# Performance work log

Measured on AMD Instinct MI355X. Metric: run time of the kernel, lower is better.

## Reference

```python
import jax, jax.numpy as jnp
import numpy as np

N = 100000
E = 1600000
D_IN, D_HID, D_OUT = 128, 256, 128


def setup_inputs() -> dict:
    key = jax.random.key(0)
    ks = jax.random.split(key, 8)
    x = jax.random.normal(ks[0], (N, D_IN), dtype=jnp.float32)
    edge_index = jax.random.randint(ks[1], (2, E), 0, N, dtype=jnp.int64)
    # PyG SAGEConv params: lin_l (applied to aggregated neighbors, has bias),
    # lin_r (applied to root/self, no bias). Stored as [in, out] for x @ W.
    s0 = 1.0 / np.sqrt(D_IN)
    s1 = 1.0 / np.sqrt(D_HID)
    Wl0 = jax.random.uniform(ks[2], (D_IN, D_HID), jnp.float32, -s0, s0)
    bl0 = jnp.zeros((D_HID,), jnp.float32)
    Wr0 = jax.random.uniform(ks[3], (D_IN, D_HID), jnp.float32, -s0, s0)
    Wl1 = jax.random.uniform(ks[4], (D_HID, D_OUT), jnp.float32, -s1, s1)
    bl1 = jnp.zeros((D_OUT,), jnp.float32)
    Wr1 = jax.random.uniform(ks[5], (D_HID, D_OUT), jnp.float32, -s1, s1)
    return {"x": x, "edge_index": edge_index, "Wl0": Wl0, "bl0": bl0,
            "Wr0": Wr0, "Wl1": Wl1, "bl1": bl1, "Wr1": Wr1}


def _sage_conv(x, src, dst, W_l, b_l, W_r, num_nodes):
    # mean-aggregate source features at destination nodes
    msg = x[src]                                         # [E, d] gather
    agg = jax.ops.segment_sum(msg, dst, num_segments=num_nodes)  # [N, d]
    deg = jax.ops.segment_sum(jnp.ones((src.shape[0],), x.dtype), dst,
                              num_segments=num_nodes)    # [N]
    agg = agg / jnp.maximum(deg, 1.0)[:, None]
    return agg @ W_l + b_l + x @ W_r                     # [N, out]


def reference(x, edge_index, Wl0, bl0, Wr0, Wl1, bl1, Wr1):
    src, dst = edge_index[0], edge_index[1]
    n = x.shape[0]
    h = _sage_conv(x, src, dst, Wl0, bl0, Wr0, n)
    h = jax.nn.relu(h)  # dropout is identity in eval mode
    out = _sage_conv(h, src, dst, Wl1, bl1, Wr1, n)
    return out
```

## Files before the change

### kernel.cpp

```cpp
#include <hip/hip_runtime.h>

typedef short bf16x8 __attribute__((ext_vector_type(8)));
typedef float f32x4 __attribute__((ext_vector_type(4)));
typedef unsigned int uint;
typedef unsigned short ushort;
typedef ushort u16x8 __attribute__((ext_vector_type(8)));
typedef uint u32x2 __attribute__((ext_vector_type(2)));
typedef uint u32x4 __attribute__((ext_vector_type(4)));

#define NBLK 256
#define LCAP 24576
#define HP 264

__device__ inline ushort f2bf(float f) {
    uint u = __builtin_bit_cast(uint, f);
    uint r = u + 0x7fffu + ((u >> 16) & 1u);
    return (ushort)(r >> 16);
}
__device__ inline float bf2f(uint lo16) {
    uint u = lo16 << 16;
    return __builtin_bit_cast(float, u);
}
__device__ inline float bf2f_hi(uint v) {
    uint u = v & 0xffff0000u;
    return __builtin_bit_cast(float, u);
}

__device__ inline void packw_body(const float* __restrict__ Wa, const float* __restrict__ Wb,
                                  ushort* __restrict__ out, int mode, int tile, int l) {
    int cb = tile >> 3, ks = tile & 7;
    int col = cb * 16 + (l & 15);
    int k0 = ks * 32 + ((l >> 4) * 8);
    ushort vals[8];
#pragma unroll
    for (int j = 0; j < 8; j++) {
        int k = k0 + j;
        float f;
        if (mode == 0)
            f = (k < 128) ? Wa[(size_t)k * 256 + col] : Wb[(size_t)(k - 128) * 256 + col];
        else
            f = (col < 128) ? Wa[(size_t)k * 128 + col] : Wb[(size_t)k * 128 + (col - 128)];
        vals[j] = f2bf(f);
    }
    ushort* dst = out + ((size_t)(ks * 16 + cb) * 64 + l) * 8;
#pragma unroll
    for (int j = 0; j < 8; j++) dst[j] = vals[j];
}

__global__ void prep_kernel(const float* __restrict__ x, ushort* __restrict__ a1,
                            const float* __restrict__ Wr0, const float* __restrict__ Wl0,
                            ushort* __restrict__ w1p,
                            const float* __restrict__ Wl1, const float* __restrict__ Wr1,
                            ushort* __restrict__ w2p,
                            const int* __restrict__ dst, int* __restrict__ ghist,
                            int E, int CE, int NB, int n) {
    __shared__ int hist[512];
    int bb = blockIdx.x;
    int tid = threadIdx.x;
    if (bb < NBLK) {
        for (int b = tid; b < NB; b += 256) hist[b] = 0;
        __syncthreads();
        int start = bb * CE, end = min(E, start + CE);
        for (int e = start + tid; e < end; e += 256) {
            int d = dst[e];
            atomicAdd(&hist[d >> 8], 1);
        }
        __syncthreads();
        for (int b = tid; b < NB; b += 256) ghist[(size_t)b * NBLK + bb] = hist[b];
    } else if (bb < NBLK + 64) {
        int r = bb - NBLK;
        int tile = (r & 31) * 4 + (tid >> 6);
        int l = tid & 63;
        if (r < 32) packw_body(Wr0, Wl0, w1p, 0, tile, l);
        else        packw_body(Wl1, Wr1, w2p, 1, tile, l);
    } else {
        int i = (bb - NBLK - 64) * 256 + tid;
        int total = n * 32;
        if (i < total) {
            int row = i >> 5, q = i & 31;
            float4 v = *(const float4*)(x + (size_t)row * 128 + q * 4);
            ushort4 o;
            o.x = f2bf(v.x); o.y = f2bf(v.y); o.z = f2bf(v.z); o.w = f2bf(v.w);
            *(ushort4*)(a1 + (size_t)row * 256 + q * 4) = o;
        }
    }
}

__global__ void scan1_kernel(const int* __restrict__ cnt, int* __restrict__ rs,
                             int* __restrict__ bsum, int n) {
    __shared__ int tmp[256];
    int tid = threadIdx.x;
    int idx = blockIdx.x * 256 + tid;
    int v = (idx < n) ? cnt[idx] : 0;
    tmp[tid] = v;
    __syncthreads();
#pragma unroll
    for (int off = 1; off < 256; off <<= 1) {
        int t = (tid >= off) ? tmp[tid - off] : 0;
        __syncthreads();
        tmp[tid] += t;
        __syncthreads();
    }
    if (idx < n) rs[idx] = tmp[tid] - v;
    if (tid == 255) bsum[blockIdx.x] = tmp[255];
}

__global__ void scan23_kernel(int* __restrict__ rs, const int* __restrict__ bsum,
                              int n, int E) {
    __shared__ int red[256];
    int tid = threadIdx.x;
    int b = blockIdx.x;
    int s = 0;
    for (int t = tid; t < b; t += 256) s += bsum[t];
    red[tid] = s;
    __syncthreads();
#pragma unroll
    for (int off = 128; off > 0; off >>= 1) {
        if (tid < off) red[tid] += red[tid + off];
        __syncthreads();
    }
    int offv = red[0];
    int idx = b * 256 + tid;
    if (idx < n) rs[idx] += offv;
    if (b == 0 && tid == 0) rs[n] = E;
}

__global__ void p3_kernel(const int* __restrict__ src, const int* __restrict__ dst,
                          const int* __restrict__ goff, uint* __restrict__ ebuck,
                          int E, int CE, int NB) {
    __shared__ int cur[512];
    int tid = threadIdx.x;
    for (int b = tid; b < NB; b += 256) cur[b] = goff[(size_t)b * NBLK + blockIdx.x];
    __syncthreads();
    int start = blockIdx.x * CE, end = min(E, start + CE);
    for (int e = start + tid; e < end; e += 256) {
        int d = dst[e];
        int s = src[e];
        int slot = atomicAdd(&cur[d >> 8], 1);
        ebuck[slot] = ((uint)(d & 255) << 17) | (uint)s;
    }
}

__global__ void p4_kernel(const uint* __restrict__ ebuck, const int* __restrict__ goff,
                          int* __restrict__ rs, int* __restrict__ nbr, int n, int E, int NB) {
    __shared__ uint ebuf[LCAP];
    __shared__ int cnt[256];
    __shared__ int cur[256];
    int tid = threadIdx.x;
    int b = blockIdx.x;
    int d0 = b << 8;
    int eb = goff[(size_t)b * NBLK];
    int ee = (b == NB - 1) ? E : goff[(size_t)(b + 1) * NBLK];
    cnt[tid] = 0;
    __syncthreads();
    int m = ee - eb;
    for (int i = tid; i < m; i += 256) {
        uint v = ebuck[eb + i];
        if (i < LCAP) ebuf[i] = v;
        atomicAdd(&cnt[v >> 17], 1);
    }
    __syncthreads();
    int v0 = cnt[tid];
    cur[tid] = v0;
    __syncthreads();
#pragma unroll
    for (int off = 1; off < 256; off <<= 1) {
        int t = (tid >= off) ? cur[tid - off] : 0;
        __syncthreads();
        cur[tid] += t;
        __syncthreads();
    }
    int excl = cur[tid] - v0;
    int node = d0 + tid;
    if (node < n) rs[node] = eb + excl;
    if (b == NB - 1 && tid == 0) rs[n] = E;
    __syncthreads();
    cur[tid] = eb + excl;
    __syncthreads();
    for (int i = tid; i < m; i += 256) {
        uint v = (i < LCAP) ? ebuf[i] : ebuck[eb + i];
        int p = atomicAdd(&cur[v >> 17], 1);
        nbr[p] = (int)(v & 0x1FFFFu);
    }
}

__launch_bounds__(512, 1)
__global__ void fused_gemm_kernel(const ushort* __restrict__ A, const ushort* __restrict__ W1,
                                  const ushort* __restrict__ W2, const float* __restrict__ b0,
                                  const float* __restrict__ b1, ushort* __restrict__ zb,
                                  float* __restrict__ outf, int n) {
    extern __shared__ ushort H[];
    int tid = threadIdx.x;
    int l = tid & 63, w = tid >> 6;
    int q = l >> 4, r16 = l & 15;
    int row0 = blockIdx.x * 128;

    {
        int rr = tid >> 5;
        int cc = (tid & 31) * 8;
#pragma unroll
        for (int it = 0; it < 8; it++) {
            int lr = it * 16 + rr;
            int row = row0 + lr;
            if (row > n - 1) row = n - 1;
            u32x4 v = *(const u32x4*)(A + (size_t)row * 256 + cc);
            *(u32x4*)(&H[(size_t)lr * HP + cc]) = v;
        }
    }

    bf16x8 bf1[2][8];
#pragma unroll
    for (int cbi = 0; cbi < 2; cbi++) {
        int cb = 2 * w + cbi;
#pragma unroll
        for (int ks = 0; ks < 8; ks++)
            bf1[cbi][ks] = *(const bf16x8*)(W1 + ((size_t)((ks * 16 + cb) * 64 + l)) * 8);
    }

    f32x4 acc[8][2];
#pragma unroll
    for (int rg = 0; rg < 8; rg++)
#pragma unroll
        for (int cbi = 0; cbi < 2; cbi++) acc[rg][cbi] = (f32x4){0.f, 0.f, 0.f, 0.f};

    __syncthreads();

#pragma unroll
    for (int rg = 0; rg < 8; rg++) {
        bf16x8 a[8];
        const ushort* hp = &H[(size_t)(rg * 16 + r16) * HP + q * 8];
#pragma unroll
        for (int ks = 0; ks < 8; ks++) a[ks] = *(const bf16x8*)(hp + ks * 32);
#pragma unroll
        for (int cbi = 0; cbi < 2; cbi++)
#pragma unroll
            for (int ks = 0; ks < 8; ks++)
                acc[rg][cbi] = __builtin_amdgcn_mfma_f32_16x16x32_bf16(bf1[cbi][ks], a[ks],
                                                                       acc[rg][cbi], 0, 0, 0);
    }

    bf16x8 bf2[2][8];
#pragma unroll
    for (int cbi = 0; cbi < 2; cbi++) {
        int cb = 2 * w + cbi;
#pragma unroll
        for (int ks = 0; ks < 8; ks++)
            bf2[cbi][ks] = *(const bf16x8*)(W2 + ((size_t)((ks * 16 + cb) * 64 + l)) * 8);
    }

    __syncthreads();

#pragma unroll
    for (int rg = 0; rg < 8; rg++) {
#pragma unroll
        for (int cbi = 0; cbi < 2; cbi++) {
            int colb = (2 * w + cbi) * 16 + q * 4;
            f32x4 bv = *(const f32x4*)(b0 + colb);
            f32x4 v = acc[rg][cbi];
            float v0 = fmaxf(v[0] + bv[0], 0.f);
            float v1 = fmaxf(v[1] + bv[1], 0.f);
            float v2 = fmaxf(v[2] + bv[2], 0.f);
            float v3 = fmaxf(v[3] + bv[3], 0.f);
            u32x2 pk;
            pk[0] = (uint)f2bf(v0) | ((uint)f2bf(v1) << 16);
            pk[1] = (uint)f2bf(v2) | ((uint)f2bf(v3) << 16);
            *(u32x2*)(&H[(size_t)(rg * 16 + r16) * HP + colb]) = pk;
            acc[rg][cbi] = (f32x4){0.f, 0.f, 0.f, 0.f};
        }
    }

    __syncthreads();

#pragma unroll
    for (int rg = 0; rg < 8; rg++) {
        bf16x8 a[8];
        const ushort* hp = &H[(size_t)(rg * 16 + r16) * HP + q * 8];
#pragma unroll
        for (int ks = 0; ks < 8; ks++) a[ks] = *(const bf16x8*)(hp + ks * 32);
#pragma unroll
        for (int cbi = 0; cbi < 2; cbi++)
#pragma unroll
            for (int ks = 0; ks < 8; ks++)
                acc[rg][cbi] = __builtin_amdgcn_mfma_f32_16x16x32_bf16(bf2[cbi][ks], a[ks],
                                                                       acc[rg][cbi], 0, 0, 0);
    }

    if (w < 4) {
#pragma unroll
        for (int rg = 0; rg < 8; rg++) {
            int row = row0 + rg * 16 + r16;
#pragma unroll
            for (int cbi = 0; cbi < 2; cbi++) {
                int colb = (2 * w + cbi) * 16 + q * 4;
                f32x4 v = acc[rg][cbi];
                u32x2 pk;
                pk[0] = (uint)f2bf(v[0]) | ((uint)f2bf(v[1]) << 16);
                pk[1] = (uint)f2bf(v[2]) | ((uint)f2bf(v[3]) << 16);
                if (row < n)
                    *(u32x2*)(zb + (size_t)row * 128 + colb) = pk;
            }
        }
    } else {
        int wq = w - 4;
#pragma unroll
        for (int rg = 0; rg < 8; rg++) {
            int row = row0 + rg * 16 + r16;
#pragma unroll
            for (int cbi = 0; cbi < 2; cbi++) {
                int colb = 32 * wq + cbi * 16 + q * 4;
                f32x4 bv = *(const f32x4*)(b1 + colb);
                f32x4 v = acc[rg][cbi];
                v[0] += bv[0]; v[1] += bv[1]; v[2] += bv[2]; v[3] += bv[3];
                if (row < n)
                    *(f32x4*)(outf + (size_t)row * 128 + colb) = v;
            }
        }
    }
}

template <int ADD>
__global__ void segmean_kernel(const uint* __restrict__ fp, int half,
                               const int* __restrict__ rs, const int* __restrict__ nbr,
                               uint* __restrict__ outb, float* __restrict__ outf, int n) {
    int w = threadIdx.x >> 6;
    int l = threadIdx.x & 63;
    int i = blockIdx.x * 4 + w;
    if (i >= n) return;
    int b = rs[i], e = rs[i + 1];
    int q = l & 31;
    int hsel = l >> 5;
    int stride2 = half >> 1;
    const uint2* fpq = (const uint2*)fp + q;
    float a0 = 0.f, a1 = 0.f, a2 = 0.f, a3 = 0.f;
    int j = b;
    for (; j + 8 <= e; j += 8) {
        int s[4];
#pragma unroll
        for (int p = 0; p < 4; p++) s[p] = nbr[j + 2 * p + hsel];
        uint2 v[4];
#pragma unroll
        for (int p = 0; p < 4; p++) v[p] = fpq[(size_t)s[p] * stride2];
#pragma unroll
        for (int p = 0; p < 4; p++) {
            a0 += bf2f(v[p].x & 0xffffu); a1 += bf2f_hi(v[p].x);
            a2 += bf2f(v[p].y & 0xffffu); a3 += bf2f_hi(v[p].y);
        }
    }
    for (; j + 2 <= e; j += 2) {
        int s = nbr[j + hsel];
        uint2 v = fpq[(size_t)s * stride2];
        a0 += bf2f(v.x & 0xffffu); a1 += bf2f_hi(v.x);
        a2 += bf2f(v.y & 0xffffu); a3 += bf2f_hi(v.y);
    }
    if (j < e && hsel == 0) {
        int s = nbr[j];
        uint2 v = fpq[(size_t)s * stride2];
        a0 += bf2f(v.x & 0xffffu); a1 += bf2f_hi(v.x);
        a2 += bf2f(v.y & 0xffffu); a3 += bf2f_hi(v.y);
    }
    a0 += __shfl_xor(a0, 32);
    a1 += __shfl_xor(a1, 32);
    a2 += __shfl_xor(a2, 32);
    a3 += __shfl_xor(a3, 32);
    if (hsel == 0) {
        int dg = e - b;
        float inv = 1.0f / (float)(dg > 1 ? dg : 1);
        a0 *= inv; a1 *= inv; a2 *= inv; a3 *= inv;
        if (ADD) {
            float* op = outf + (size_t)i * (2 * half) + q * 4;
            f32x4 o = *(const f32x4*)op;
            o[0] += a0; o[1] += a1; o[2] += a2; o[3] += a3;
            *(f32x4*)op = o;
        } else {
            u32x2 pk;
            pk[0] = (uint)f2bf(a0) | ((uint)f2bf(a1) << 16);
            pk[1] = (uint)f2bf(a2) | ((uint)f2bf(a3) << 16);
            *(u32x2*)(outb + (size_t)i * half + q * 2) = pk;
        }
    }
}


extern "C" void kernel_launch(void* const* d_in, const int* in_sizes, int n_in,
                              void* d_out, int out_size, void* d_ws, size_t ws_size,
                              hipStream_t stream) {
    const float* x = (const float*)d_in[0];
    const int* ei = (const int*)d_in[1];
    const float* Wl0 = (const float*)d_in[2];
    const float* bl0 = (const float*)d_in[3];
    const float* Wr0 = (const float*)d_in[4];
    const float* Wl1 = (const float*)d_in[5];
    const float* bl1 = (const float*)d_in[6];
    const float* Wr1 = (const float*)d_in[7];
    float* outp = (float*)d_out;

    int n = in_sizes[0] / 128;
    int E = in_sizes[1] / 2;
    const int* srcv = ei;
    const int* dstv = ei + E;

    int NB = (n + 255) >> 8;
    int NG = NB * NBLK;
    int CE = (E + NBLK - 1) / NBLK;

    char* w = (char*)d_ws;
    auto align = [](size_t v) { return (v + 255) & ~(size_t)255; };
    size_t off = 0;
    int* rs    = (int*)(w + off); off = align(off + (size_t)(n + 1) * 4);
    int* bsum2 = (int*)(w + off); off = align(off + (size_t)512 * 4);
    int* ghist = (int*)(w + off); off = align(off + (size_t)(NG + 1) * 4);
    int* goff  = (int*)(w + off); off = align(off + (size_t)(NG + 1) * 4);
    uint* ebuck = (uint*)(w + off); off = align(off + (size_t)E * 4);
    int* nbr   = (int*)(w + off); off = align(off + (size_t)E * 4);
    ushort* a1  = (ushort*)(w + off); off = align(off + (size_t)n * 256 * 2);
    ushort* zb  = (ushort*)(w + off); off = align(off + (size_t)n * 128 * 2);
    ushort* w1p = (ushort*)(w + off); off = align(off + (size_t)256 * 256 * 2);
    ushort* w2p = (ushort*)(w + off); off = align(off + (size_t)256 * 256 * 2);
    (void)ws_size; (void)n_in; (void)out_size;

    int nb2 = (NG + 255) / 256;
    int ncx = (n * 32 + 255) / 256;

    prep_kernel<<<NBLK + 64 + ncx, 256, 0, stream>>>(x, a1, Wr0, Wl0, w1p, Wl1, Wr1, w2p,
                                                     dstv, ghist, E, CE, NB, n);
    scan1_kernel<<<nb2, 256, 0, stream>>>(ghist, goff, bsum2, NG);
    scan23_kernel<<<nb2, 256, 0, stream>>>(goff, bsum2, NG, E);
    p3_kernel<<<NBLK, 256, 0, stream>>>(srcv, dstv, goff, ebuck, E, CE, NB);
    p4_kernel<<<NB, 256, 0, stream>>>(ebuck, goff, rs, nbr, n, E, NB);

    int segb = (n + 3) / 4;
    int mb = (n + 127) / 128;
    int ldsz = 128 * HP * 2;

    hipFuncSetAttribute((const void*)fused_gemm_kernel,
                        hipFuncAttributeMaxDynamicSharedMemorySize, ldsz);

    segmean_kernel<0><<<segb, 256, 0, stream>>>((const uint*)a1, 128, rs, nbr,
                                                (uint*)(a1 + 128), nullptr, n);
    fused_gemm_kernel<<<mb, 512, ldsz, stream>>>(a1, w1p, w2p, bl0, bl1, zb, outp, n);
    segmean_kernel<1><<<segb, 256, 0, stream>>>((const uint*)zb, 64, rs, nbr,
                                                nullptr, outp, n);
}
```

Measured before the change: 248.6 us.

## Store node features in column-sliced layout so gathers hit compact per-slice tables

Node feature tables (bf16 x, aggregated x, and layer-2 projections) are now stored as eight 16-column slices, each laid out as [n][16]. The segment-mean kernel gives each block one slice, with four lanes per node, so concurrent gathers touch a 3.2MB table that can stay in cache instead of scattering across full 256B rows. The fused GEMM loads from and writes to this sliced layout. In exchange, each gather now reads only 32B per neighbor, nbr and rs are re-read eight times (once per slice), and the lanes within a wave handle nodes with different degrees, which causes divergence.

After: 295.2 us. 18.7% more time.

```diff
diff --git a/kernel.cpp b/kernel.cpp
--- a/kernel.cpp
+++ b/kernel.cpp
@@ -4,7 +4,6 @@
 typedef float f32x4 __attribute__((ext_vector_type(4)));
 typedef unsigned int uint;
 typedef unsigned short ushort;
-typedef ushort u16x8 __attribute__((ext_vector_type(8)));
 typedef uint u32x2 __attribute__((ext_vector_type(2)));
 typedef uint u32x4 __attribute__((ext_vector_type(4)));
 
@@ -47,7 +46,7 @@
     for (int j = 0; j < 8; j++) dst[j] = vals[j];
 }
 
-__global__ void prep_kernel(const float* __restrict__ x, ushort* __restrict__ a1,
+__global__ void prep_kernel(const float* __restrict__ x, ushort* __restrict__ xsl,
                             const float* __restrict__ Wr0, const float* __restrict__ Wl0,
                             ushort* __restrict__ w1p,
                             const float* __restrict__ Wl1, const float* __restrict__ Wr1,
@@ -74,14 +73,22 @@
         if (r < 32) packw_body(Wr0, Wl0, w1p, 0, tile, l);
         else        packw_body(Wl1, Wr1, w2p, 1, tile, l);
     } else {
-        int i = (bb - NBLK - 64) * 256 + tid;
-        int total = n * 32;
-        if (i < total) {
-            int row = i >> 5, q = i & 31;
-            float4 v = *(const float4*)(x + (size_t)row * 128 + q * 4);
-            ushort4 o;
-            o.x = f2bf(v.x); o.y = f2bf(v.y); o.z = f2bf(v.z); o.w = f2bf(v.w);
-            *(ushort4*)(a1 + (size_t)row * 256 + q * 4) = o;
+        int row = (bb - NBLK - 64) * 256 + tid;
+        if (row < n) {
+            const float* xr = x + (size_t)row * 128;
+#pragma unroll
+            for (int c = 0; c < 8; c++) {
+                ushort h[16];
+#pragma unroll
+                for (int m = 0; m < 4; m++) {
+                    float4 f = *(const float4*)(xr + c * 16 + m * 4);
+                    h[m * 4 + 0] = f2bf(f.x); h[m * 4 + 1] = f2bf(f.y);
+                    h[m * 4 + 2] = f2bf(f.z); h[m * 4 + 3] = f2bf(f.w);
+                }
+                ushort* dp = xsl + ((size_t)c * n + row) * 16;
+                *(u32x4*)dp = *(const u32x4*)&h[0];
+                *(u32x4*)(dp + 8) = *(const u32x4*)&h[8];
+            }
         }
     }
 }
@@ -185,10 +192,10 @@
 }
 
 __launch_bounds__(512, 1)
-__global__ void fused_gemm_kernel(const ushort* __restrict__ A, const ushort* __restrict__ W1,
-                                  const ushort* __restrict__ W2, const float* __restrict__ b0,
-                                  const float* __restrict__ b1, ushort* __restrict__ zb,
-                                  float* __restrict__ outf, int n) {
+__global__ void fused_gemm_kernel(const ushort* __restrict__ xsl, const ushort* __restrict__ asl,
+                                  const ushort* __restrict__ W1, const ushort* __restrict__ W2,
+                                  const float* __restrict__ b0, const float* __restrict__ b1,
+                                  ushort* __restrict__ zsl, float* __restrict__ outf, int n) {
     extern __shared__ ushort H[];
     int tid = threadIdx.x;
     int l = tid & 63, w = tid >> 6;
@@ -196,15 +203,16 @@
     int row0 = blockIdx.x * 128;
 
     {
-        int rr = tid >> 5;
-        int cc = (tid & 31) * 8;
-#pragma unroll
-        for (int it = 0; it < 8; it++) {
-            int lr = it * 16 + rr;
-            int row = row0 + lr;
-            if (row > n - 1) row = n - 1;
-            u32x4 v = *(const u32x4*)(A + (size_t)row * 256 + cc);
-            *(u32x4*)(&H[(size_t)lr * HP + cc]) = v;
+        int row = tid >> 2;
+        int ql = tid & 3;
+        int grow = row0 + row;
+        if (grow > n - 1) grow = n - 1;
+#pragma unroll
+        for (int s = 0; s < 16; s++) {
+            const ushort* src = (s < 8) ? (xsl + ((size_t)s * n + grow) * 16)
+                                        : (asl + ((size_t)(s - 8) * n + grow) * 16);
+            uint2 v = *(const uint2*)(src + ql * 4);
+            *(uint2*)(&H[(size_t)row * HP + s * 16 + ql * 4]) = v;
         }
     }
 
@@ -291,13 +299,13 @@
             int row = row0 + rg * 16 + r16;
 #pragma unroll
             for (int cbi = 0; cbi < 2; cbi++) {
-                int colb = (2 * w + cbi) * 16 + q * 4;
+                int slice = 2 * w + cbi;
                 f32x4 v = acc[rg][cbi];
                 u32x2 pk;
                 pk[0] = (uint)f2bf(v[0]) | ((uint)f2bf(v[1]) << 16);
                 pk[1] = (uint)f2bf(v[2]) | ((uint)f2bf(v[3]) << 16);
                 if (row < n)
-                    *(u32x2*)(zb + (size_t)row * 128 + colb) = pk;
+                    *(u32x2*)(zsl + ((size_t)slice * n + row) * 16 + q * 4) = pk;
             }
         }
     } else {
@@ -319,64 +327,49 @@
 }
 
 template <int ADD>
-__global__ void segmean_kernel(const uint* __restrict__ fp, int half,
-                               const int* __restrict__ rs, const int* __restrict__ nbr,
-                               uint* __restrict__ outb, float* __restrict__ outf, int n) {
-    int w = threadIdx.x >> 6;
-    int l = threadIdx.x & 63;
-    int i = blockIdx.x * 4 + w;
+__global__ void segmean_kernel(const ushort* __restrict__ tbl, const int* __restrict__ rs,
+                               const int* __restrict__ nbr, ushort* __restrict__ outb,
+                               float* __restrict__ outf, int n) {
+    int tid = threadIdx.x;
+    int c = blockIdx.x & 7;
+    int i = (blockIdx.x >> 3) * 64 + (tid >> 2);
     if (i >= n) return;
+    int ql = tid & 3;
     int b = rs[i], e = rs[i + 1];
-    int q = l & 31;
-    int hsel = l >> 5;
-    int stride2 = half >> 1;
-    const uint2* fpq = (const uint2*)fp + q;
+    const ushort* tb = tbl + ((size_t)c * n) * 16 + ql * 4;
     float a0 = 0.f, a1 = 0.f, a2 = 0.f, a3 = 0.f;
     int j = b;
-    for (; j + 8 <= e; j += 8) {
-        int s[4];
-#pragma unroll
-        for (int p = 0; p < 4; p++) s[p] = nbr[j + 2 * p + hsel];
-        uint2 v[4];
-#pragma unroll
-        for (int p = 0; p < 4; p++) v[p] = fpq[(size_t)s[p] * stride2];
-#pragma unroll
-        for (int p = 0; p < 4; p++) {
-            a0 += bf2f(v[p].x & 0xffffu); a1 += bf2f_hi(v[p].x);
-            a2 += bf2f(v[p].y & 0xffffu); a3 += bf2f_hi(v[p].y);
-        }
-    }
-    for (; j + 2 <= e; j += 2) {
-        int s = nbr[j + hsel];
-        uint2 v = fpq[(size_t)s * stride2];
-        a0 += bf2f(v.x & 0xffffu); a1 += bf2f_hi(v.x);
-        a2 += bf2f(v.y & 0xffffu); a3 += bf2f_hi(v.y);
-    }
-    if (j < e && hsel == 0) {
-        int s = nbr[j];
-        uint2 v = fpq[(size_t)s * stride2];
-        a0 += bf2f(v.x & 0xffffu); a1 += bf2f_hi(v.x);
-        a2 += bf2f(v.y & 0xffffu); a3 += bf2f_hi(v.y);
-    }
-    a0 += __shfl_xor(a0, 32);
-    a1 += __shfl_xor(a1, 32);
-    a2 += __shfl_xor(a2, 32);
-    a3 += __shfl_xor(a3, 32);
-    if (hsel == 0) {
-        int dg = e - b;
-        float inv = 1.0f / (float)(dg > 1 ? dg : 1);
-        a0 *= inv; a1 *= inv; a2 *= inv; a3 *= inv;
-        if (ADD) {
-            float* op = outf + (size_t)i * (2 * half) + q * 4;
-            f32x4 o = *(const f32x4*)op;
-            o[0] += a0; o[1] += a1; o[2] += a2; o[3] += a3;
-            *(f32x4*)op = o;
-        } else {
-            u32x2 pk;
-            pk[0] = (uint)f2bf(a0) | ((uint)f2bf(a1) << 16);
-            pk[1] = (uint)f2bf(a2) | ((uint)f2bf(a3) << 16);
-            *(u32x2*)(outb + (size_t)i * half + q * 2) = pk;
-        }
+    for (; j + 4 <= e; j += 4) {
+        int s0 = nbr[j], s1 = nbr[j + 1], s2 = nbr[j + 2], s3 = nbr[j + 3];
+        uint2 v0 = *(const uint2*)(tb + (size_t)s0 * 16);
+        uint2 v1 = *(const uint2*)(tb + (size_t)s1 * 16);
+        uint2 v2 = *(const uint2*)(tb + (size_t)s2 * 16);
+        uint2 v3 = *(const uint2*)(tb + (size_t)s3 * 16);
+        a0 += bf2f(v0.x & 0xffffu) + bf2f(v1.x & 0xffffu) + bf2f(v2.x & 0xffffu) + bf2f(v3.x & 0xffffu);
+        a1 += bf2f_hi(v0.x) + bf2f_hi(v1.x) + bf2f_hi(v2.x) + bf2f_hi(v3.x);
+        a2 += bf2f(v0.y & 0xffffu) + bf2f(v1.y & 0xffffu) + bf2f(v2.y & 0xffffu) + bf2f(v3.y & 0xffffu);
+        a3 += bf2f_hi(v0.y) + bf2f_hi(v1.y) + bf2f_hi(v2.y) + bf2f_hi(v3.y);
+    }
+    for (; j < e; j++) {
+        uint2 v = *(const uint2*)(tb + (size_t)nbr[j] * 16);
+        a0 += bf2f(v.x & 0xffffu);
+        a1 += bf2f_hi(v.x);
+        a2 += bf2f(v.y & 0xffffu);
+        a3 += bf2f_hi(v.y);
+    }
+    int dg = e - b;
+    float inv = 1.0f / (float)(dg > 1 ? dg : 1);
+    a0 *= inv; a1 *= inv; a2 *= inv; a3 *= inv;
+    if (ADD) {
+        float* op = outf + (size_t)i * 128 + c * 16 + ql * 4;
+        f32x4 o = *(const f32x4*)op;
+        o[0] += a0; o[1] += a1; o[2] += a2; o[3] += a3;
+        *(f32x4*)op = o;
+    } else {
+        u32x2 pk;
+        pk[0] = (uint)f2bf(a0) | ((uint)f2bf(a1) << 16);
+        pk[1] = (uint)f2bf(a2) | ((uint)f2bf(a3) << 16);
+        *(u32x2*)(outb + ((size_t)c * n + i) * 16 + ql * 4) = pk;
     }
 }
 
@@ -412,32 +405,31 @@
     int* goff  = (int*)(w + off); off = align(off + (size_t)(NG + 1) * 4);
     uint* ebuck = (uint*)(w + off); off = align(off + (size_t)E * 4);
     int* nbr   = (int*)(w + off); off = align(off + (size_t)E * 4);
-    ushort* a1  = (ushort*)(w + off); off = align(off + (size_t)n * 256 * 2);
-    ushort* zb  = (ushort*)(w + off); off = align(off + (size_t)n * 128 * 2);
+    ushort* xsl = (ushort*)(w + off); off = align(off + (size_t)n * 128 * 2);
+    ushort* asl = (ushort*)(w + off); off = align(off + (size_t)n * 128 * 2);
+    ushort* zsl = (ushort*)(w + off); off = align(off + (size_t)n * 128 * 2);
     ushort* w1p = (ushort*)(w + off); off = align(off + (size_t)256 * 256 * 2);
     ushort* w2p = (ushort*)(w + off); off = align(off + (size_t)256 * 256 * 2);
     (void)ws_size; (void)n_in; (void)out_size;
 
     int nb2 = (NG + 255) / 256;
-    int ncx = (n * 32 + 255) / 256;
-
-    prep_kernel<<<NBLK + 64 + ncx, 256, 0, stream>>>(x, a1, Wr0, Wl0, w1p, Wl1, Wr1, w2p,
+    int ncx = (n + 255) / 256;
+
+    prep_kernel<<<NBLK + 64 + ncx, 256, 0, stream>>>(x, xsl, Wr0, Wl0, w1p, Wl1, Wr1, w2p,
                                                      dstv, ghist, E, CE, NB, n);
     scan1_kernel<<<nb2, 256, 0, stream>>>(ghist, goff, bsum2, NG);
     scan23_kernel<<<nb2, 256, 0, stream>>>(goff, bsum2, NG, E);
     p3_kernel<<<NBLK, 256, 0, stream>>>(srcv, dstv, goff, ebuck, E, CE, NB);
     p4_kernel<<<NB, 256, 0, stream>>>(ebuck, goff, rs, nbr, n, E, NB);
 
-    int segb = (n + 3) / 4;
+    int segb = ((n + 63) / 64) * 8;
     int mb = (n + 127) / 128;
     int ldsz = 128 * HP * 2;
 
     hipFuncSetAttribute((const void*)fused_gemm_kernel,
                         hipFuncAttributeMaxDynamicSharedMemorySize, ldsz);
 
-    segmean_kernel<0><<<segb, 256, 0, stream>>>((const uint*)a1, 128, rs, nbr,
-                                                (uint*)(a1 + 128), nullptr, n);
-    fused_gemm_kernel<<<mb, 512, ldsz, stream>>>(a1, w1p, w2p, bl0, bl1, zb, outp, n);
-    segmean_kernel<1><<<segb, 256, 0, stream>>>((const uint*)zb, 64, rs, nbr,
-                                                nullptr, outp, n);
-}
+    segmean_kernel<0><<<segb, 256, 0, stream>>>(xsl, rs, nbr, asl, nullptr, n);
+    fused_gemm_kernel<<<mb, 512, ldsz, stream>>>(xsl, asl, w1p, w2p, bl0, bl1, zsl, outp, n);
+    segmean_kernel<1><<<segb, 256, 0, stream>>>(zsl, rs, nbr, nullptr, outp, n);
+}
```
